# Kernel tuning notes

Hardware: AMD Instinct MI355X
Metric: run time of the kernel (lower is better)

Reference implementation:

```python
import jax, jax.numpy as jnp
import numpy as np

BN_EPS = 1e-5
W_BITS = 2
A_BITS = 2


def _quantize_k(x, k):
    # uniform quantization of x in [0,1] to k bits, straight-through estimator
    n = float(2 ** k - 1)
    q = jnp.round(x * n) / n
    return x + jax.lax.stop_gradient(q - x)


def _quant_weight(w, k):
    # DoReFa-style weight quantization to [-1, 1]
    t = jnp.tanh(w)
    t = t / (2.0 * jnp.max(jnp.abs(t))) + 0.5
    return 2.0 * _quantize_k(t, k) - 1.0


def _quant_act(x, k):
    # DoReFa-style activation quantization: clamp to [0,1], quantize
    return _quantize_k(jnp.clip(x, 0.0, 1.0), k)


def _conv3x3(x, w, stride=1):
    # x: [N,C,H,W], w: [O,I,3,3], padding=1
    return jax.lax.conv_general_dilated(
        x, w, window_strides=(stride, stride), padding=((1, 1), (1, 1)),
        dimension_numbers=('NCHW', 'OIHW', 'NCHW'))


def _bn(x, gamma, beta, mean, var):
    inv = gamma / jnp.sqrt(var + BN_EPS)           # [C]
    return x * inv[None, :, None, None] + (beta - mean * inv)[None, :, None, None]


def setup_inputs() -> dict:
    key = jax.random.key(0)
    ks = jax.random.split(key, 8)
    N, C, H, W = 64, 256, 28, 28
    x = jax.random.normal(ks[0], (N, C, H, W), dtype=jnp.float32)
    w1 = jax.random.normal(ks[1], (C, C, 3, 3), dtype=jnp.float32) * 0.05
    w2 = jax.random.normal(ks[2], (C, C, 3, 3), dtype=jnp.float32) * 0.05
    g1 = jnp.ones((C,), jnp.float32)
    b1 = jnp.zeros((C,), jnp.float32)
    m1 = jax.random.normal(ks[3], (C,), dtype=jnp.float32) * 0.1
    v1 = jax.random.uniform(ks[4], (C,), dtype=jnp.float32) + 0.5
    g2 = jnp.ones((C,), jnp.float32)
    b2 = jnp.zeros((C,), jnp.float32)
    m2 = jax.random.normal(ks[5], (C,), dtype=jnp.float32) * 0.1
    v2 = jax.random.uniform(ks[6], (C,), dtype=jnp.float32) + 0.5
    return {'x': x, 'w1': w1, 'g1': g1, 'b1': b1, 'm1': m1, 'v1': v1,
            'w2': w2, 'g2': g2, 'b2': b2, 'm2': m2, 'v2': v2}


def reference(x, w1, g1, b1, m1, v1, w2, g2, b2, m2, v2):
    residual = x
    # conv1 (2-bit quantized weights & activations) -> bn1 -> relu
    out = _conv3x3(_quant_act(x, A_BITS), _quant_weight(w1, W_BITS), stride=1)
    out = jax.nn.relu(_bn(out, g1, b1, m1, v1))
    # conv2 (2-bit quantized) -> bn2
    out = _conv3x3(_quant_act(out, A_BITS), _quant_weight(w2, W_BITS), stride=1)
    out = _bn(out, g2, b2, m2, v2)
    # residual add + relu
    return jax.nn.relu(out + residual)
```

## Files before the change

### kernel.cpp

```cpp
#include <hip/hip_runtime.h>


#define ABUF 14745600
using i32x4 = __attribute__((ext_vector_type(4))) int;

__device__ __forceinline__ void gload16(const void* g, void* l) {
  typedef const __attribute__((address_space(1))) unsigned int* gp_t;
  typedef __attribute__((address_space(3))) unsigned int* lp_t;
  __builtin_amdgcn_global_load_lds((gp_t)g, (lp_t)l, 16, 0, 0);
}

__device__ __forceinline__ int border_pix(int bp) {
  int hh, ww;
  if (bp < 30)      { hh = 0;       ww = bp; }
  else if (bp < 60) { hh = 29;      ww = bp - 30; }
  else if (bp < 88) { hh = bp - 59; ww = 0; }
  else              { hh = bp - 87; ww = 29; }
  return hh * 30 + ww;
}

__global__ void pre_k(const float* __restrict__ x, unsigned char* __restrict__ a1,
                      unsigned char* __restrict__ a2T,
                      const float* __restrict__ w1, const float* __restrict__ w2,
                      float* __restrict__ partial,
                      const float* g1, const float* b1, const float* m1, const float* v1,
                      const float* g2, const float* b2, const float* m2, const float* v2,
                      float* s1, float* t1, float* s2, float* t2) {
  const int t = threadIdx.x;
  if (blockIdx.x >= 256) {
    int bx = blockIdx.x - 256;
    int ten = bx >> 6, bxl = bx & 63;
    if (ten == 0 && bxl == 0) {
      float i1 = g1[t] / sqrtf(v1[t] + 1e-5f);
      s1[t] = i1 * (1.f / 9.f);
      t1[t] = b1[t] - m1[t] * i1;
      float i2 = g2[t] / sqrtf(v2[t] + 1e-5f);
      s2[t] = i2 * (1.f / 9.f);
      t2[t] = b2[t] - m2[t] * i2;
    }
    const float4* v = (const float4*)(ten ? w2 : w1);
    float loc = 0.f;
    for (int i = bxl * 256 + t; i < 147456; i += 16384) {
      float4 f = v[i];
      loc = fmaxf(loc, fmaxf(fmaxf(fabsf(f.x), fabsf(f.y)), fmaxf(fabsf(f.z), fabsf(f.w))));
    }
    #pragma unroll
    for (int off = 32; off; off >>= 1) loc = fmaxf(loc, __shfl_xor(loc, off));
    __shared__ float red[4];
    if ((t & 63) == 0) red[t >> 6] = loc;
    __syncthreads();
    if (t == 0)
      partial[ten * 64 + bxl] = fmaxf(fmaxf(red[0], red[1]), fmaxf(red[2], red[3]));
    return;
  }
  __shared__ unsigned au[784 * 17];
  const int n = blockIdx.x >> 2, cq = blockIdx.x & 3;
  const int c4 = t >> 4, q = t & 15;

  #pragma unroll
  for (int m = 0; m < 2; ++m) {
    int s2i = t + m * 256;
    if (s2i < 464) {
      int bp = s2i >> 2, quad = s2i & 3;
      uint4 z = {0, 0, 0, 0};
      *(uint4*)(a1 + ((size_t)n * 900 + border_pix(bp)) * 256 + cq * 64 + quad * 16) = z;
    }
  }
  #pragma unroll
  for (int m = 0; m < 2; ++m) {
    int s2i = t + m * 256;
    if (s2i < 464) {
      int bp = s2i >> 2, sl = cq * 4 + (s2i & 3);
      uint4 z = {0, 0, 0, 0};
      *(uint4*)(a2T + ((size_t)sl * 57600 + n * 900 + border_pix(bp)) * 16) = z;
    }
  }

  const float* xb = x + (size_t)n * 200704 + (cq * 64 + c4 * 4) * 784;
  #pragma unroll
  for (int k = 0; k < 13; ++k) {
    int hw4 = q + k * 16;
    if (hw4 < 196) {
      unsigned b[4][4];
      #pragma unroll
      for (int i = 0; i < 4; ++i) {
        float4 f = *(const float4*)(xb + i * 784 + hw4 * 4);
        b[i][0] = (unsigned)(int)rintf(3.f * fminf(fmaxf(f.x, 0.f), 1.f));
        b[i][1] = (unsigned)(int)rintf(3.f * fminf(fmaxf(f.y, 0.f), 1.f));
        b[i][2] = (unsigned)(int)rintf(3.f * fminf(fmaxf(f.z, 0.f), 1.f));
        b[i][3] = (unsigned)(int)rintf(3.f * fminf(fmaxf(f.w, 0.f), 1.f));
      }
      #pragma unroll
      for (int j = 0; j < 4; ++j)
        au[(hw4 * 4 + j) * 17 + c4] = b[0][j] | (b[1][j] << 8) | (b[2][j] << 16) | (b[3][j] << 24);
    }
  }
  __syncthreads();
  #pragma unroll
  for (int m = 0; m < 13; ++m) {
    int s = t + m * 256;
    if (s < 3136) {
      int pix = s >> 2, quad = s & 3;
      uint4 v;
      v.x = au[pix * 17 + quad * 4 + 0];
      v.y = au[pix * 17 + quad * 4 + 1];
      v.z = au[pix * 17 + quad * 4 + 2];
      v.w = au[pix * 17 + quad * 4 + 3];
      int hh = pix / 28, ww = pix - hh * 28;
      *(uint4*)(a1 + (((n * 30 + hh + 1) * 30) + ww + 1) * 256 + cq * 64 + quad * 16) = v;
    }
  }
}

__global__ void wquant_k(const float* __restrict__ w1, const float* __restrict__ w2,
                         const float* __restrict__ partial,
                         unsigned char* __restrict__ wqT1, unsigned char* __restrict__ wq2) {
  const int oo = blockIdx.x, ten = blockIdx.y;
  const float* w = ten ? w2 : w1;
  __shared__ float wl[2304];
  const int t = threadIdx.x;
  float pm = partial[ten * 64 + (t & 63)];
  #pragma unroll
  for (int off = 32; off; off >>= 1) pm = fmaxf(pm, __shfl_xor(pm, off));
  const float inv = 1.f / (2.f * tanhf(pm));
  #pragma unroll
  for (int k = 0; k < 9; ++k) wl[k * 256 + t] = tanhf(w[oo * 2304 + k * 256 + t]);
  __syncthreads();
  #pragma unroll
  for (int k = 0; k < 9; ++k) {
    int j = k * 256 + t, t9 = j >> 8, ci = j & 255;
    float tt = wl[ci * 9 + t9] * inv + 0.5f;
    int q = (int)rintf(tt * 3.f);
    unsigned char val = (unsigned char)(signed char)(2 * q - 3);
    if (ten == 0)
      wqT1[(t9 * 16 + (ci >> 4)) * 4096 + oo * 16 + (ci & 15)] = val;
    else
      wq2[oo * 2304 + j] = val;
  }
}

#define LGKM0() do { asm volatile("s_waitcnt lgkmcnt(0)" ::: "memory"); \
  __builtin_amdgcn_sched_barrier(0); } while (0)
#define SP1() __builtin_amdgcn_s_setprio(1)
#define SP0() __builtin_amdgcn_s_setprio(0)

template <int MODE>
__global__ __launch_bounds__(512, 2) void conv_gemm(
    const unsigned char* __restrict__ actA,
    const unsigned char* __restrict__ bsrc,
    const float* __restrict__ sC, const float* __restrict__ tC,
    const float* __restrict__ xres, unsigned char* __restrict__ actout,
    float* __restrict__ fout) {
  extern __shared__ __align__(16) char lds[];
  const int tid = threadIdx.x, wv = tid >> 6, lane = tid & 63;
  const int bswz = blockIdx.x & 7, bloc = blockIdx.x >> 3;
  const int wg = (bswz < 4 ? bswz * 25 : 100 + (bswz - 4) * 24) + bloc;
  const int pixBase = wg * 256;
  const int wvm = wv >> 2, wvn = wv & 3;
  const bool grpB = (wvm == 1);

  int aB[2][2];
  {
    int s = (lane & 7) ^ ((lane >> 3) & 7);
    #pragma unroll
    for (int h = 0; h < 2; ++h)
      #pragma unroll
      for (int c = 0; c < 2; ++c) {
        int r = h * 128 + c * 64 + wv * 8 + (lane >> 3);
        if (MODE == 0) {
          int p = pixBase + r;
          int n = p / 784, rem = p % 784, hh = rem / 28, ww = rem % 28;
          aB[h][c] = (((n * 30 + hh) * 30 + ww) << 8) + (s << 4);
        } else {
          aB[h][c] = r * 2304 + (s << 4);
        }
      }
  }
  auto tofA = [](int kt) {
    int tap = kt >> 1;
    return ((tap / 3) * 30 + (tap % 3)) * 256 + ((kt & 1) << 7);
  };
  auto stageA = [&](int kt) {
    const int koff = (MODE == 0) ? tofA(kt) : kt * 128;
    #pragma unroll
    for (int h = 0; h < 2; ++h) {
      const int base = (kt & 1) * 32768 + h * 16384 + wv * 1024;
      gload16(actA + aB[h][0] + koff, &lds[base]);
      gload16(actA + aB[h][1] + koff, &lds[base + 8192]);
    }
  };

  int bB[4];
  #pragma unroll
  for (int q = 0; q < 4; ++q) {
    if (MODE == 0) {
      int ch = wvn * 64 + q * 16 + (lane & 15);
      bB[q] = ch * 16 + (lane >> 4) * 4096;
    } else {
      int p = pixBase + wvn * 64 + q * 16 + (lane & 15);
      int n = p / 784, rem = p % 784, hh = rem / 28, ww = rem % 28;
      bB[q] = (n * 900 + hh * 30 + ww) * 16 + (lane >> 4) * 921600;
    }
  }
  i32x4 bc[4][2];
  auto loadB = [&](int kt) {
    const int tap = kt >> 1;
    #pragma unroll
    for (int q = 0; q < 4; ++q)
      #pragma unroll
      for (int kc = 0; kc < 2; ++kc) {
        int off;
        if (MODE == 0)
          off = bB[q] + kt * 32768 + kc * 16384;
        else
          off = bB[q] + ((kt & 1) * 8 + kc * 4) * 921600 +
                ((tap / 3) * 30 + (tap % 3)) * 16;
        bc[q][kc] = *(const i32x4*)(bsrc + off);
      }
  };

  i32x4 acc[8][4];
  #pragma unroll
  for (int i = 0; i < 8; ++i)
    #pragma unroll
    for (int j = 0; j < 4; ++j) acc[i][j] = (i32x4){0, 0, 0, 0};
  i32x4 pa[4][2];

  auto rdA = [&](int buf, int mh) {
    #pragma unroll
    for (int f = 0; f < 4; ++f) {
      int r = wvm * 128 + mh * 64 + f * 16 + (lane & 15);
      int rb = buf * 32768 + r * 128;
      #pragma unroll
      for (int kc = 0; kc < 2; ++kc) {
        int sl = kc * 4 + (lane >> 4);
        pa[f][kc] = *(const i32x4*)&lds[rb + ((sl ^ (r & 7)) << 4)];
      }
    }
  };
  auto quad = [&](int mh, int nh) {
    #pragma unroll
    for (int kc = 0; kc < 2; ++kc)
      #pragma unroll
      for (int f = 0; f < 4; ++f)
        #pragma unroll
        for (int g = 0; g < 2; ++g)
          acc[mh * 4 + f][nh * 2 + g] = __builtin_amdgcn_mfma_i32_16x16x64_i8(
              pa[f][kc], bc[nh * 2 + g][kc], acc[mh * 4 + f][nh * 2 + g], 0, 0, 0);
  };

  stageA(0);
  asm volatile("s_waitcnt vmcnt(0)" ::: "memory");
  __builtin_amdgcn_sched_barrier(0);
  __builtin_amdgcn_s_barrier();

  for (int t = 0; t < 18; ++t) {
    const int buf = t & 1;
    if (t > 0) {
      asm volatile("s_waitcnt vmcnt(0) lgkmcnt(0)" ::: "memory");
      __builtin_amdgcn_sched_barrier(0);
      __builtin_amdgcn_s_barrier();
      __builtin_amdgcn_sched_barrier(0);
    }
    if (t <= 16) stageA(t + 1);
    if (grpB && t > 0) {
      SP1(); quad(1, 0); quad(1, 1); SP0();
    }
    loadB(t);
    rdA(buf, 0);
    LGKM0();
    SP1(); quad(0, 0); quad(0, 1); SP0();
    rdA(buf, 1);
    LGKM0();
    if (!grpB) { SP1(); quad(1, 0); quad(1, 1); SP0(); }
  }
  if (grpB) { SP1(); quad(1, 0); quad(1, 1); SP0(); }

  if (MODE == 0) {
    float sj[4], tj[4];
    #pragma unroll
    for (int j = 0; j < 4; ++j) {
      int c = wvn * 64 + j * 16 + (lane & 15);
      sj[j] = sC[c]; tj[j] = tC[c];
    }
    __syncthreads();
    #pragma unroll
    for (int i = 0; i < 8; ++i) {
      int lp0 = wvm * 128 + i * 16 + ((lane >> 4) << 2);
      #pragma unroll
      for (int j = 0; j < 4; ++j) {
        int lch = wvn * 64 + j * 16 + (lane & 15);
        #pragma unroll
        for (int r = 0; r < 4; ++r) {
          float y = (float)acc[i][j][r] * sj[j] + tj[j];
          y = fminf(fmaxf(y, 0.f), 1.f);
          int lp = lp0 + r;
          lds[lp * 256 + (lch ^ ((lp & 7) << 4))] = (char)(int)rintf(y * 3.f);
        }
      }
    }
    __syncthreads();
    int rr = tid >> 1, hf = tid & 1;
    int p = pixBase + rr;
    int n = p / 784, rem = p % 784, hh = rem / 28, ww = rem % 28;
    int pixpad = n * 900 + (hh + 1) * 30 + (ww + 1);
    #pragma unroll
    for (int k = 0; k < 8; ++k) {
      uint4 v = *(const uint4*)&lds[rr * 256 + ((hf * 128 + k * 16) ^ ((rr & 7) << 4))];
      *(uint4*)(actout + (size_t)(hf * 8 + k) * 921600 + pixpad * 16) = v;
    }
  } else {
    #pragma unroll
    for (int i = 0; i < 8; ++i) {
      int c = wvm * 128 + i * 16 + ((lane >> 4) << 2) + (lane & 3);
      float sc = sC[c], tc = tC[c];
      #pragma unroll
      for (int j = 0; j < 4; ++j) {
        int a0 = acc[i][j][0], a1 = acc[i][j][1], a2 = acc[i][j][2], a3 = acc[i][j][3];
        int t0 = __builtin_amdgcn_mov_dpp(a0, 0xB1, 0xF, 0xF, true);
        int t1 = __builtin_amdgcn_mov_dpp(a1, 0xB1, 0xF, 0xF, true);
        int t2 = __builtin_amdgcn_mov_dpp(a2, 0xB1, 0xF, 0xF, true);
        int t3 = __builtin_amdgcn_mov_dpp(a3, 0xB1, 0xF, 0xF, true);
        const bool o1 = (lane & 1) != 0;
        int v0 = o1 ? t1 : a0;
        int v1 = o1 ? a1 : t0;
        int v2 = o1 ? t3 : a2;
        int v3 = o1 ? a3 : t2;
        int u0 = __builtin_amdgcn_mov_dpp(v2, 0x4E, 0xF, 0xF, true);
        int u1 = __builtin_amdgcn_mov_dpp(v3, 0x4E, 0xF, 0xF, true);
        int u2 = __builtin_amdgcn_mov_dpp(v0, 0x4E, 0xF, 0xF, true);
        int u3 = __builtin_amdgcn_mov_dpp(v1, 0x4E, 0xF, 0xF, true);
        const bool o2 = (lane & 2) != 0;
        int z0 = o2 ? u0 : v0;
        int z1 = o2 ? u1 : v1;
        int z2 = o2 ? v2 : u2;
        int z3 = o2 ? v3 : u3;
        int P = pixBase + wvn * 64 + j * 16 + (lane & 12);
        int n = P / 784, rem = P - n * 784;
        size_t addr = (size_t)n * 200704 + (size_t)c * 784 + rem;
        float4 xr = *(const float4*)(xres + addr);
        float4 y;
        y.x = fmaxf((float)z0 * sc + tc + xr.x, 0.f);
        y.y = fmaxf((float)z1 * sc + tc + xr.y, 0.f);
        y.z = fmaxf((float)z2 * sc + tc + xr.z, 0.f);
        y.w = fmaxf((float)z3 * sc + tc + xr.w, 0.f);
        *(float4*)(fout + addr) = y;
      }
    }
  }
}

extern "C" void kernel_launch(void* const* d_in, const int* in_sizes, int n_in,
                              void* d_out, int out_size, void* d_ws, size_t ws_size,
                              hipStream_t stream) {
  const float* x  = (const float*)d_in[0];
  const float* w1 = (const float*)d_in[1];
  const float* g1 = (const float*)d_in[2];
  const float* b1 = (const float*)d_in[3];
  const float* m1 = (const float*)d_in[4];
  const float* v1 = (const float*)d_in[5];
  const float* w2 = (const float*)d_in[6];
  const float* g2 = (const float*)d_in[7];
  const float* b2 = (const float*)d_in[8];
  const float* m2 = (const float*)d_in[9];
  const float* v2 = (const float*)d_in[10];

  char* ws = (char*)d_ws;
  float* partial = (float*)ws;
  float* s1 = (float*)(ws + 1024);
  float* t1 = (float*)(ws + 2048);
  float* s2 = (float*)(ws + 3072);
  float* t2 = (float*)(ws + 4096);
  unsigned char* a1  = (unsigned char*)(ws + 8192);
  unsigned char* a2T = a1 + ABUF;
  unsigned char* wqT1 = a2T + ABUF;
  unsigned char* wq2  = wqT1 + 589824;

  void (*k0)(const unsigned char*, const unsigned char*, const float*, const float*,
             const float*, unsigned char*, float*) = conv_gemm<0>;
  void (*k1)(const unsigned char*, const unsigned char*, const float*, const float*,
             const float*, unsigned char*, float*) = conv_gemm<1>;
  (void)hipFuncSetAttribute((const void*)k0, hipFuncAttributeMaxDynamicSharedMemorySize, 65536);
  (void)hipFuncSetAttribute((const void*)k1, hipFuncAttributeMaxDynamicSharedMemorySize, 65536);

  pre_k<<<384, 256, 0, stream>>>(x, a1, a2T, w1, w2, partial,
                                 g1, b1, m1, v1, g2, b2, m2, v2, s1, t1, s2, t2);
  wquant_k<<<dim3(256, 2), 256, 0, stream>>>(w1, w2, partial, wqT1, wq2);
  conv_gemm<0><<<196, 512, 65536, stream>>>(a1, wqT1, s1, t1, nullptr, a2T, nullptr);
  conv_gemm<1><<<196, 512, 65536, stream>>>(wq2, a2T, s2, t2,
                                            x, nullptr, (float*)d_out);
}
```

Measured before the change: 206.3 us.

## Shrink conv GEMM tiles to 128x128 with 256-thread blocks and 784-block grid

Replaces the 256x256 output tile per 512-thread block (196 blocks, less than one per CU on 256 CUs) with 128x128 tiles per 256-thread block (784 blocks), splitting output channels across blocks via chBase. The main loop is simplified to issue the next A stage, load B, read A and run all MFMAs, then barrier, dropping the staggered wave-group scheduling. The goal is to fill all CUs and raise occupancy with smaller LDS use. In exchange, each block reuses A and B less, so global traffic per MFMA rises.

```diff
diff --git a/kernel.cpp b/kernel.cpp
--- a/kernel.cpp
+++ b/kernel.cpp
@@ -145,7 +145,7 @@
 #define SP0() __builtin_amdgcn_s_setprio(0)
 
 template <int MODE>
-__global__ __launch_bounds__(512, 2) void conv_gemm(
+__global__ __launch_bounds__(256, 3) void conv_gemm(
     const unsigned char* __restrict__ actA,
     const unsigned char* __restrict__ bsrc,
     const float* __restrict__ sC, const float* __restrict__ tC,
@@ -153,28 +153,25 @@
     float* __restrict__ fout) {
   extern __shared__ __align__(16) char lds[];
   const int tid = threadIdx.x, wv = tid >> 6, lane = tid & 63;
-  const int bswz = blockIdx.x & 7, bloc = blockIdx.x >> 3;
-  const int wg = (bswz < 4 ? bswz * 25 : 100 + (bswz - 4) * 24) + bloc;
-  const int pixBase = wg * 256;
-  const int wvm = wv >> 2, wvn = wv & 3;
-  const bool grpB = (wvm == 1);
-
-  int aB[2][2];
+  const int wg = (blockIdx.x & 7) * 98 + (blockIdx.x >> 3);
+  const int by = wg / 392, bx = wg - by * 392;
+  const int pixBase = bx * 128, chBase = by * 128;
+  const int wvm = wv >> 1, wvn = wv & 1;
+
+  int aB[4];
   {
     int s = (lane & 7) ^ ((lane >> 3) & 7);
     #pragma unroll
-    for (int h = 0; h < 2; ++h)
-      #pragma unroll
-      for (int c = 0; c < 2; ++c) {
-        int r = h * 128 + c * 64 + wv * 8 + (lane >> 3);
-        if (MODE == 0) {
-          int p = pixBase + r;
-          int n = p / 784, rem = p % 784, hh = rem / 28, ww = rem % 28;
-          aB[h][c] = (((n * 30 + hh) * 30 + ww) << 8) + (s << 4);
-        } else {
-          aB[h][c] = r * 2304 + (s << 4);
-        }
-      }
+    for (int c8 = 0; c8 < 4; ++c8) {
+      int r = c8 * 32 + wv * 8 + (lane >> 3);
+      if (MODE == 0) {
+        int p = pixBase + r;
+        int n = p / 784, rem = p % 784, hh = rem / 28, ww = rem % 28;
+        aB[c8] = (((n * 30 + hh) * 30 + ww) << 8) + (s << 4);
+      } else {
+        aB[c8] = (chBase + r) * 2304 + (s << 4);
+      }
+    }
   }
   auto tofA = [](int kt) {
     int tap = kt >> 1;
@@ -182,19 +179,17 @@
   };
   auto stageA = [&](int kt) {
     const int koff = (MODE == 0) ? tofA(kt) : kt * 128;
-    #pragma unroll
-    for (int h = 0; h < 2; ++h) {
-      const int base = (kt & 1) * 32768 + h * 16384 + wv * 1024;
-      gload16(actA + aB[h][0] + koff, &lds[base]);
-      gload16(actA + aB[h][1] + koff, &lds[base + 8192]);
-    }
+    const int base = (kt & 1) * 16384 + wv * 1024;
+    #pragma unroll
+    for (int c8 = 0; c8 < 4; ++c8)
+      gload16(actA + aB[c8] + koff, &lds[base + c8 * 4096]);
   };
 
   int bB[4];
   #pragma unroll
   for (int q = 0; q < 4; ++q) {
     if (MODE == 0) {
-      int ch = wvn * 64 + q * 16 + (lane & 15);
+      int ch = chBase + wvn * 64 + q * 16 + (lane & 15);
       bB[q] = ch * 16 + (lane >> 4) * 4096;
     } else {
       int p = pixBase + wvn * 64 + q * 16 + (lane & 15);
@@ -202,35 +197,33 @@
       bB[q] = (n * 900 + hh * 30 + ww) * 16 + (lane >> 4) * 921600;
     }
   }
-  i32x4 bc[4][2];
-  auto loadB = [&](int kt) {
+  i32x4 bc0[4], bc1[4];
+  auto loadB = [&](int kt, int kc, i32x4* bc) {
     const int tap = kt >> 1;
     #pragma unroll
-    for (int q = 0; q < 4; ++q)
-      #pragma unroll
-      for (int kc = 0; kc < 2; ++kc) {
-        int off;
-        if (MODE == 0)
-          off = bB[q] + kt * 32768 + kc * 16384;
-        else
-          off = bB[q] + ((kt & 1) * 8 + kc * 4) * 921600 +
-                ((tap / 3) * 30 + (tap % 3)) * 16;
-        bc[q][kc] = *(const i32x4*)(bsrc + off);
-      }
-  };
-
-  i32x4 acc[8][4];
-  #pragma unroll
-  for (int i = 0; i < 8; ++i)
+    for (int q = 0; q < 4; ++q) {
+      int off;
+      if (MODE == 0)
+        off = bB[q] + kt * 32768 + kc * 16384;
+      else
+        off = bB[q] + ((kt & 1) * 8 + kc * 4) * 921600 +
+              ((tap / 3) * 30 + (tap % 3)) * 16;
+      bc[q] = *(const i32x4*)(bsrc + off);
+    }
+  };
+
+  i32x4 acc[4][4];
+  #pragma unroll
+  for (int i = 0; i < 4; ++i)
     #pragma unroll
     for (int j = 0; j < 4; ++j) acc[i][j] = (i32x4){0, 0, 0, 0};
   i32x4 pa[4][2];
 
-  auto rdA = [&](int buf, int mh) {
+  auto rdA = [&](int buf) {
     #pragma unroll
     for (int f = 0; f < 4; ++f) {
-      int r = wvm * 128 + mh * 64 + f * 16 + (lane & 15);
-      int rb = buf * 32768 + r * 128;
+      int r = wvm * 64 + f * 16 + (lane & 15);
+      int rb = buf * 16384 + r * 128;
       #pragma unroll
       for (int kc = 0; kc < 2; ++kc) {
         int sl = kc * 4 + (lane >> 4);
@@ -238,15 +231,13 @@
       }
     }
   };
-  auto quad = [&](int mh, int nh) {
-    #pragma unroll
-    for (int kc = 0; kc < 2; ++kc)
-      #pragma unroll
-      for (int f = 0; f < 4; ++f)
-        #pragma unroll
-        for (int g = 0; g < 2; ++g)
-          acc[mh * 4 + f][nh * 2 + g] = __builtin_amdgcn_mfma_i32_16x16x64_i8(
-              pa[f][kc], bc[nh * 2 + g][kc], acc[mh * 4 + f][nh * 2 + g], 0, 0, 0);
+  auto halfK = [&](int kc, i32x4* bc) {
+    #pragma unroll
+    for (int f = 0; f < 4; ++f)
+      #pragma unroll
+      for (int g = 0; g < 4; ++g)
+        acc[f][g] = __builtin_amdgcn_mfma_i32_16x16x64_i8(
+            pa[f][kc], bc[g], acc[f][g], 0, 0, 0);
   };
 
   stageA(0);
@@ -256,37 +247,31 @@
 
   for (int t = 0; t < 18; ++t) {
     const int buf = t & 1;
-    if (t > 0) {
+    if (t < 17) stageA(t + 1);
+    loadB(t, 0, bc0);
+    loadB(t, 1, bc1);
+    rdA(buf);
+    LGKM0();
+    SP1(); halfK(0, bc0); halfK(1, bc1); SP0();
+    if (t < 17) {
       asm volatile("s_waitcnt vmcnt(0) lgkmcnt(0)" ::: "memory");
       __builtin_amdgcn_sched_barrier(0);
       __builtin_amdgcn_s_barrier();
       __builtin_amdgcn_sched_barrier(0);
     }
-    if (t <= 16) stageA(t + 1);
-    if (grpB && t > 0) {
-      SP1(); quad(1, 0); quad(1, 1); SP0();
-    }
-    loadB(t);
-    rdA(buf, 0);
-    LGKM0();
-    SP1(); quad(0, 0); quad(0, 1); SP0();
-    rdA(buf, 1);
-    LGKM0();
-    if (!grpB) { SP1(); quad(1, 0); quad(1, 1); SP0(); }
-  }
-  if (grpB) { SP1(); quad(1, 0); quad(1, 1); SP0(); }
+  }
 
   if (MODE == 0) {
     float sj[4], tj[4];
     #pragma unroll
     for (int j = 0; j < 4; ++j) {
-      int c = wvn * 64 + j * 16 + (lane & 15);
+      int c = chBase + wvn * 64 + j * 16 + (lane & 15);
       sj[j] = sC[c]; tj[j] = tC[c];
     }
     __syncthreads();
     #pragma unroll
-    for (int i = 0; i < 8; ++i) {
-      int lp0 = wvm * 128 + i * 16 + ((lane >> 4) << 2);
+    for (int i = 0; i < 4; ++i) {
+      int lp0 = wvm * 64 + i * 16 + ((lane >> 4) << 2);
       #pragma unroll
       for (int j = 0; j < 4; ++j) {
         int lch = wvn * 64 + j * 16 + (lane & 15);
@@ -295,7 +280,7 @@
           float y = (float)acc[i][j][r] * sj[j] + tj[j];
           y = fminf(fmaxf(y, 0.f), 1.f);
           int lp = lp0 + r;
-          lds[lp * 256 + (lch ^ ((lp & 7) << 4))] = (char)(int)rintf(y * 3.f);
+          lds[lp * 128 + (lch ^ ((lp & 7) << 4))] = (char)(int)rintf(y * 3.f);
         }
       }
     }
@@ -305,14 +290,15 @@
     int n = p / 784, rem = p % 784, hh = rem / 28, ww = rem % 28;
     int pixpad = n * 900 + (hh + 1) * 30 + (ww + 1);
     #pragma unroll
-    for (int k = 0; k < 8; ++k) {
-      uint4 v = *(const uint4*)&lds[rr * 256 + ((hf * 128 + k * 16) ^ ((rr & 7) << 4))];
-      *(uint4*)(actout + (size_t)(hf * 8 + k) * 921600 + pixpad * 16) = v;
+    for (int k = 0; k < 4; ++k) {
+      int m = hf * 4 + k;
+      uint4 v = *(const uint4*)&lds[rr * 128 + ((m << 4) ^ ((rr & 7) << 4))];
+      *(uint4*)(actout + (size_t)(by * 8 + m) * 921600 + pixpad * 16) = v;
     }
   } else {
     #pragma unroll
-    for (int i = 0; i < 8; ++i) {
-      int c = wvm * 128 + i * 16 + ((lane >> 4) << 2) + (lane & 3);
+    for (int i = 0; i < 4; ++i) {
+      int c = chBase + wvm * 64 + i * 16 + ((lane >> 4) << 2) + (lane & 3);
       float sc = sC[c], tc = tC[c];
       #pragma unroll
       for (int j = 0; j < 4; ++j) {
@@ -380,13 +366,13 @@
              const float*, unsigned char*, float*) = conv_gemm<0>;
   void (*k1)(const unsigned char*, const unsigned char*, const float*, const float*,
              const float*, unsigned char*, float*) = conv_gemm<1>;
-  (void)hipFuncSetAttribute((const void*)k0, hipFuncAttributeMaxDynamicSharedMemorySize, 65536);
-  (void)hipFuncSetAttribute((const void*)k1, hipFuncAttributeMaxDynamicSharedMemorySize, 65536);
+  (void)hipFuncSetAttribute((const void*)k0, hipFuncAttributeMaxDynamicSharedMemorySize, 32768);
+  (void)hipFuncSetAttribute((const void*)k1, hipFuncAttributeMaxDynamicSharedMemorySize, 32768);
 
   pre_k<<<384, 256, 0, stream>>>(x, a1, a2T, w1, w2, partial,
                                  g1, b1, m1, v1, g2, b2, m2, v2, s1, t1, s2, t2);
   wquant_k<<<dim3(256, 2), 256, 0, stream>>>(w1, w2, partial, wqT1, wq2);
-  conv_gemm<0><<<196, 512, 65536, stream>>>(a1, wqT1, s1, t1, nullptr, a2T, nullptr);
-  conv_gemm<1><<<196, 512, 65536, stream>>>(wq2, a2T, s2, t2,
+  conv_gemm<0><<<784, 256, 32768, stream>>>(a1, wqT1, s1, t1, nullptr, a2T, nullptr);
+  conv_gemm<1><<<784, 256, 32768, stream>>>(wq2, a2T, s2, t2,
                                             x, nullptr, (float*)d_out);
 }
```

After: 218.2 us. 5.8% more time.
